# Performance work log

Measured on AMD Instinct MI355X. Metric: run time of the kernel, lower is better.

The kernel has to match this reference:

```python
import jax, jax.numpy as jnp
import numpy as np

DIM = 256
NUM_HEADS = 8
SAMPLE_RATIO = 4
B, H, W = 8, 32, 32
HEAD_DIM = DIM // NUM_HEADS
SCALE = HEAD_DIM ** (-0.5)


def conv1x1(x, w, b):
    # x: [B,C,H,W], w: [O,C], b: [O]  (1x1 conv == per-pixel channel matmul)
    return jnp.einsum('bchw,oc->bohw', x, w) + b[None, :, None, None]


def setup_inputs() -> dict:
    key = jax.random.key(0)
    ks = jax.random.split(key, 16)
    s = 0.02
    x = jax.random.normal(ks[0], (B, DIM, H, W), dtype=jnp.float32)
    # gumbel noise for the two gumbel-softmax gates (sampled once, fed as input)
    u_q = jax.random.uniform(ks[1], (B, SAMPLE_RATIO, H, W), minval=1e-6, maxval=1.0 - 1e-6)
    u_k = jax.random.uniform(ks[2], (B, SAMPLE_RATIO, H, W), minval=1e-6, maxval=1.0 - 1e-6)
    g_q = -jnp.log(-jnp.log(u_q))
    g_k = -jnp.log(-jnp.log(u_k))
    return {
        'x': x,
        'g_q': g_q,
        'g_k': g_k,
        'Wsq': jax.random.normal(ks[3], (SAMPLE_RATIO, DIM)) * s,
        'bsq': jnp.zeros((SAMPLE_RATIO,), jnp.float32),
        'Wsk': jax.random.normal(ks[4], (SAMPLE_RATIO, DIM)) * s,
        'bsk': jnp.zeros((SAMPLE_RATIO,), jnp.float32),
        'Wq': jax.random.normal(ks[5], (DIM, DIM)) * s,
        'bq': jnp.zeros((DIM,), jnp.float32),
        'Wk': jax.random.normal(ks[6], (DIM, DIM)) * s,
        'bk': jnp.zeros((DIM,), jnp.float32),
        'Wv': jax.random.normal(ks[7], (DIM, DIM)) * s,
        'bv': jnp.zeros((DIM,), jnp.float32),
        'Wp': jax.random.normal(ks[8], (DIM, DIM)) * s,
        'bp': jnp.zeros((DIM,), jnp.float32),
    }


def reference(x, g_q, g_k, Wsq, bsq, Wsk, bsk, Wq, bq, Wk, bk, Wv, bv, Wp, bp):
    Bn, C, Hh, Ww = x.shape
    N = Hh * Ww
    # gumbel-softmax (soft, tau=1) gates; keep channel 0 only
    sample_q = jax.nn.softmax(conv1x1(x, Wsq, bsq) + g_q, axis=1)[:, :1]   # [B,1,H,W]
    sample_k = jax.nn.softmax(conv1x1(x, Wsk, bsk) + g_k, axis=1)[:, :1]

    q = (sample_q * conv1x1(x, Wq, bq)).reshape(Bn, NUM_HEADS, HEAD_DIM, N)
    k = (sample_k * conv1x1(x, Wk, bk)).reshape(Bn, NUM_HEADS, HEAD_DIM, N)
    v_full = conv1x1(x, Wv, bv)                                            # shortcut [B,C,H,W]
    v = v_full.reshape(Bn, NUM_HEADS, HEAD_DIM, N)

    # dense attention: scores [B,h,N,N]
    attn = jax.nn.softmax(jnp.einsum('bhdn,bhdm->bhnm', q * SCALE, k), axis=-1)
    out = jnp.einsum('bhnm,bhdm->bhdn', attn, v).reshape(Bn, C, Hh, Ww)

    gated = sample_q * out + (1.0 - sample_q) * v_full
    return conv1x1(gated, Wp, bp)
```

## Files before the change

### kernel.cpp

```cpp
#include <hip/hip_runtime.h>
#include <hip/hip_bf16.h>

typedef __hip_bfloat16 bf16;
typedef __attribute__((ext_vector_type(8))) short short8;
typedef __attribute__((ext_vector_type(4))) short sh4;
typedef __attribute__((ext_vector_type(4))) float f32x4;

static __device__ __forceinline__ float bf2f(bf16 h) { return __bfloat162float(h); }
static __device__ __forceinline__ short f2bfs(float f) {
    bf16 h = __float2bfloat16(f);
    return *reinterpret_cast<short*>(&h);
}
static __device__ __forceinline__ short8 cvt8(float4 a, float4 b) {
    short8 o;
    o[0] = f2bfs(a.x); o[1] = f2bfs(a.y); o[2] = f2bfs(a.z); o[3] = f2bfs(a.w);
    o[4] = f2bfs(b.x); o[5] = f2bfs(b.y); o[6] = f2bfs(b.z); o[7] = f2bfs(b.w);
    return o;
}

constexpr int Bn = 8;
constexpr int C  = 256;
constexpr int N  = 1024;
constexpr int NH = 8;
constexpr int HD = 32;
constexpr int TS = 264;
constexpr float SCALE = 0.17677669529663687f;

__global__ __launch_bounds__(256) void k_prep(
    const float* __restrict__ Wq, const float* __restrict__ Wk,
    const float* __restrict__ Wv, const float* __restrict__ Wp,
    bf16* __restrict__ Wb)
{
    const int tid = threadIdx.x;
    const int mat = blockIdx.x >> 2, seg = blockIdx.x & 3;
    const float* src = (mat == 0) ? Wq : (mat == 1) ? Wk : (mat == 2) ? Wv : Wp;
    short* dst = reinterpret_cast<short*>(Wb) + (size_t)mat * 256 * 256;
#pragma unroll
    for (int i = 0; i < 16; ++i) {
        int f4 = seg * 4096 + i * 256 + tid;
        float4 v = reinterpret_cast<const float4*>(src)[f4];
        sh4 o;
        o[0] = f2bfs(v.x); o[1] = f2bfs(v.y); o[2] = f2bfs(v.z); o[3] = f2bfs(v.w);
        *reinterpret_cast<sh4*>(dst + (size_t)f4 * 4) = o;
    }
}

__global__ __launch_bounds__(256) void k_fused5(
    const float* __restrict__ x, const float* __restrict__ gq, const float* __restrict__ gk,
    const float* __restrict__ Wsq, const float* __restrict__ bsq,
    const float* __restrict__ Wsk, const float* __restrict__ bsk,
    const bf16* __restrict__ Wb,
    const float* __restrict__ bq, const float* __restrict__ bk, const float* __restrict__ bv,
    bf16* __restrict__ qo, bf16* __restrict__ ko, bf16* __restrict__ vo,
    float* __restrict__ sqg)
{
    __shared__ short T[64 * TS];
    __shared__ float sq_lds[64];
    __shared__ float sk_lds[64];

    const int tid  = threadIdx.x;
    const int wave = tid >> 6;
    const int lane = tid & 63;
    const int col  = lane & 15;
    const int quad = lane >> 4;

    const int b    = blockIdx.x >> 6;
    const int rest = blockIdx.x & 63;
    const int n0   = (rest >> 2) * 64;
    const int mq   = rest & 3;

    {
        const float* xp = x + (size_t)b * C * N + n0;
        const int row = tid >> 4;
        const int f   = tid & 15;
#pragma unroll
        for (int p = 0; p < 16; ++p) {
            int c = p * 16 + row;
            float4 v = *reinterpret_cast<const float4*>(xp + (size_t)c * N + f * 4);
            T[(f * 4 + 0) * TS + c] = f2bfs(v.x);
            T[(f * 4 + 1) * TS + c] = f2bfs(v.y);
            T[(f * 4 + 2) * TS + c] = f2bfs(v.z);
            T[(f * 4 + 3) * TS + c] = f2bfs(v.w);
        }
    }
    __syncthreads();

    if (wave == 0) {
        const float* wsrc = (col < 4) ? (Wsq + col * C) : (Wsk + (col & 3) * C);
        f32x4 ga[4] = {};
#pragma unroll
        for (int k0 = 0; k0 < 256; k0 += 32) {
            float4 w0 = *reinterpret_cast<const float4*>(wsrc + k0 + quad * 8);
            float4 w1 = *reinterpret_cast<const float4*>(wsrc + k0 + quad * 8 + 4);
            short8 af = cvt8(w0, w1);
#pragma unroll
            for (int cf = 0; cf < 4; ++cf) {
                short8 bfr = *reinterpret_cast<const short8*>(&T[(cf * 16 + col) * TS + k0 + quad * 8]);
                ga[cf] = __builtin_amdgcn_mfma_f32_16x16x32_bf16(af, bfr, ga[cf], 0, 0, 0);
            }
        }
        if (quad < 2) {
            const float* bsrc = (quad == 0) ? bsq : bsk;
            const float* gsrc = (quad == 0) ? gq : gk;
#pragma unroll
            for (int cf = 0; cf < 4; ++cf) {
                int n = n0 + cf * 16 + col;
                float a[4];
#pragma unroll
                for (int r = 0; r < 4; ++r)
                    a[r] = ga[cf][r] + bsrc[r] + gsrc[(size_t)b * 4 * N + (size_t)r * N + n];
                float mx = fmaxf(fmaxf(a[0], a[1]), fmaxf(a[2], a[3]));
                float e = 0.f;
#pragma unroll
                for (int r = 0; r < 4; ++r) e += __expf(a[r] - mx);
                float p0 = __expf(a[0] - mx) / e;
                if (quad == 0) {
                    sq_lds[cf * 16 + col] = p0;
                    if (mq == 0) sqg[b * N + n] = p0;
                } else {
                    sk_lds[cf * 16 + col] = p0;
                }
            }
        }
    }
    __syncthreads();

    const short* Ws = reinterpret_cast<const short*>(Wb);
    const int mbase = mq * 192 + wave * 48;
    f32x4 acc[3][4] = {};
#pragma unroll
    for (int k0 = 0; k0 < 256; k0 += 32) {
        short8 bfr[4];
#pragma unroll
        for (int cf = 0; cf < 4; ++cf)
            bfr[cf] = *reinterpret_cast<const short8*>(&T[(cf * 16 + col) * TS + k0 + quad * 8]);
#pragma unroll
        for (int i = 0; i < 3; ++i) {
            int m = mbase + i * 16;
            const short* wr = Ws + (size_t)(m >> 8) * 65536
                              + (size_t)((m & 255) + col) * 256 + k0 + quad * 8;
            short8 af = *reinterpret_cast<const short8*>(wr);
#pragma unroll
            for (int cf = 0; cf < 4; ++cf)
                acc[i][cf] = __builtin_amdgcn_mfma_f32_16x16x32_bf16(af, bfr[cf], acc[i][cf], 0, 0, 0);
        }
    }
#pragma unroll
    for (int i = 0; i < 3; ++i) {
        int m = mbase + i * 16;
        int mat = m >> 8;
        int cr  = (m & 255) + quad * 4;
        const float* bb = (mat == 0) ? bq : (mat == 1) ? bk : bv;
        float bias[4];
#pragma unroll
        for (int r = 0; r < 4; ++r) bias[r] = bb[cr + r];
        if (mat < 2) {
            short* op = reinterpret_cast<short*>((mat == 0) ? qo : ko) + (size_t)b * N * C;
#pragma unroll
            for (int cf = 0; cf < 4; ++cf) {
                int n = n0 + cf * 16 + col;
                float g = (mat == 0) ? sq_lds[cf * 16 + col] * SCALE
                                     : sk_lds[cf * 16 + col];
                sh4 pack;
#pragma unroll
                for (int r = 0; r < 4; ++r) pack[r] = f2bfs((acc[i][cf][r] + bias[r]) * g);
                *reinterpret_cast<sh4*>(op + (size_t)n * C + cr) = pack;
            }
        } else {
            bf16* op = vo + (size_t)b * C * N;
#pragma unroll
            for (int cf = 0; cf < 4; ++cf) {
                int n = n0 + cf * 16 + col;
#pragma unroll
                for (int r = 0; r < 4; ++r)
                    op[(size_t)(cr + r) * N + n] = __float2bfloat16(acc[i][cf][r] + bias[r]);
            }
        }
    }
}

__global__ __launch_bounds__(256) void k_attn5(
    const bf16* __restrict__ qo, const bf16* __restrict__ ko,
    const bf16* __restrict__ vo, const float* __restrict__ sqg,
    bf16* __restrict__ gt)
{
    __shared__ short P_lds[4][32 * 72];

    const int tid  = threadIdx.x;
    const int wave = tid >> 6;
    const int lane = tid & 63;
    const int col  = lane & 15;
    const int quad = lane >> 4;

    const int b = blockIdx.x >> 6;
    const int h = (blockIdx.x >> 3) & 7;
    const int qbase = (blockIdx.x & 7) * 128 + wave * 32;

    const short* kp = reinterpret_cast<const short*>(ko) + (size_t)b * N * C + h * HD + quad * 8;
    const short* vp = reinterpret_cast<const short*>(vo) + (size_t)b * C * N + (size_t)h * HD * N;

    short8 qf[2];
    {
        const short* qp = reinterpret_cast<const short*>(qo) + (size_t)b * N * C + h * HD + quad * 8;
#pragma unroll
        for (int g = 0; g < 2; ++g)
            qf[g] = *reinterpret_cast<const short8*>(qp + (size_t)(qbase + g * 16 + col) * C);
    }

    float l[2] = {};
    f32x4 oac[2][2] = {};
    short* P = P_lds[wave];

    short8 kf[4];
#pragma unroll
    for (int c = 0; c < 4; ++c)
        kf[c] = *reinterpret_cast<const short8*>(kp + (size_t)(c * 16 + col) * C);

    for (int kb = 0; kb < N; kb += 64) {
        short8 vf[2][2];
#pragma unroll
        for (int kg = 0; kg < 2; ++kg)
#pragma unroll
            for (int dh = 0; dh < 2; ++dh)
                vf[kg][dh] = *reinterpret_cast<const short8*>(vp + (size_t)(dh * 16 + col) * N + kb + kg * 32 + quad * 8);

#pragma unroll
        for (int g = 0; g < 2; ++g) {
            float s[16];
#pragma unroll
            for (int c = 0; c < 4; ++c) {
                f32x4 acc = {};
                acc = __builtin_amdgcn_mfma_f32_16x16x32_bf16(kf[c], qf[g], acc, 0, 0, 0);
#pragma unroll
                for (int r = 0; r < 4; ++r) s[c * 4 + r] = acc[r];
            }
            float p[16], lloc = 0.f;
#pragma unroll
            for (int i = 0; i < 16; ++i) { p[i] = __expf(s[i]); lloc += p[i]; }
            lloc += __shfl_xor(lloc, 16, 64);
            lloc += __shfl_xor(lloc, 32, 64);
            l[g] += lloc;
#pragma unroll
            for (int c = 0; c < 4; ++c) {
                sh4 pk;
#pragma unroll
                for (int r = 0; r < 4; ++r) pk[r] = f2bfs(p[c * 4 + r]);
                *reinterpret_cast<sh4*>(&P[(g * 16 + col) * 72 + c * 16 + quad * 4]) = pk;
            }
        }

        const int kn = (kb + 64) & (N - 1);
#pragma unroll
        for (int c = 0; c < 4; ++c)
            kf[c] = *reinterpret_cast<const short8*>(kp + (size_t)(kn + c * 16 + col) * C);

#pragma unroll
        for (int kg = 0; kg < 2; ++kg) {
#pragma unroll
            for (int g = 0; g < 2; ++g) {
                short8 pf = *reinterpret_cast<const short8*>(&P[(g * 16 + col) * 72 + kg * 32 + quad * 8]);
#pragma unroll
                for (int dh = 0; dh < 2; ++dh)
                    oac[g][dh] = __builtin_amdgcn_mfma_f32_16x16x32_bf16(vf[kg][dh], pf, oac[g][dh], 0, 0, 0);
            }
        }
    }

#pragma unroll
    for (int g = 0; g < 2; ++g) {
        const int q = qbase + g * 16 + col;
        const float invl = 1.f / l[g];
        const float sqv  = sqg[b * N + q];
        const float hv   = 1.f - sqv;
        short* gp = reinterpret_cast<short*>(gt) + ((size_t)b * N + q) * C + h * HD + quad * 4;
#pragma unroll
        for (int dh = 0; dh < 2; ++dh) {
            sh4 pack;
#pragma unroll
            for (int r = 0; r < 4; ++r) {
                int d = dh * 16 + quad * 4 + r;
                float vb = bf2f(*reinterpret_cast<const bf16*>(vp + (size_t)d * N + q));
                pack[r] = f2bfs(sqv * (oac[g][dh][r] * invl) + hv * vb);
            }
            *reinterpret_cast<sh4*>(gp + dh * 16) = pack;
        }
    }
}

__global__ __launch_bounds__(256) void k_projm3(
    const bf16* __restrict__ gt, const bf16* __restrict__ Wpb,
    const float* __restrict__ bp, float* __restrict__ out)
{
    const int tid  = threadIdx.x;
    const int wave = tid >> 6, lane = tid & 63;
    const int col  = lane & 15, quad = lane >> 4;
    const int mrow = blockIdx.x * 128 + wave * 32;
    const int b    = blockIdx.z;
    const int n0   = blockIdx.y * 32;

    const short* Wm = reinterpret_cast<const short*>(Wpb);
    const short* gp = reinterpret_cast<const short*>(gt) + (size_t)b * N * C;

    f32x4 acc[2][2] = {};
#pragma unroll
    for (int k0 = 0; k0 < 256; k0 += 32) {
        short8 af[2];
#pragma unroll
        for (int mi = 0; mi < 2; ++mi)
            af[mi] = *reinterpret_cast<const short8*>(Wm + (size_t)(mrow + mi * 16 + col) * 256 + k0 + quad * 8);
        short8 bfr[2];
#pragma unroll
        for (int cf = 0; cf < 2; ++cf)
            bfr[cf] = *reinterpret_cast<const short8*>(gp + (size_t)(n0 + cf * 16 + col) * C + k0 + quad * 8);
#pragma unroll
        for (int mi = 0; mi < 2; ++mi)
#pragma unroll
            for (int cf = 0; cf < 2; ++cf)
                acc[mi][cf] = __builtin_amdgcn_mfma_f32_16x16x32_bf16(af[mi], bfr[cf], acc[mi][cf], 0, 0, 0);
    }

    float* op = out + (size_t)b * C * N;
#pragma unroll
    for (int mi = 0; mi < 2; ++mi) {
        int cr = mrow + mi * 16 + quad * 4;
        float bias[4];
#pragma unroll
        for (int r = 0; r < 4; ++r) bias[r] = bp[cr + r];
#pragma unroll
        for (int cf = 0; cf < 2; ++cf) {
            int n = n0 + cf * 16 + col;
#pragma unroll
            for (int r = 0; r < 4; ++r)
                op[(size_t)(cr + r) * N + n] = acc[mi][cf][r] + bias[r];
        }
    }
}

extern "C" void kernel_launch(void* const* d_in, const int* in_sizes, int n_in,
                              void* d_out, int out_size, void* d_ws, size_t ws_size,
                              hipStream_t stream)
{
    const float* x   = (const float*)d_in[0];
    const float* gq  = (const float*)d_in[1];
    const float* gk  = (const float*)d_in[2];
    const float* Wsq = (const float*)d_in[3];
    const float* bsq = (const float*)d_in[4];
    const float* Wsk = (const float*)d_in[5];
    const float* bsk = (const float*)d_in[6];
    const float* Wq  = (const float*)d_in[7];
    const float* bq  = (const float*)d_in[8];
    const float* Wk  = (const float*)d_in[9];
    const float* bk  = (const float*)d_in[10];
    const float* Wv  = (const float*)d_in[11];
    const float* bv  = (const float*)d_in[12];
    const float* Wp  = (const float*)d_in[13];
    const float* bp  = (const float*)d_in[14];

    char* ws = (char*)d_ws;
    float* sqg = (float*)ws;
    bf16* Wb   = (bf16*)(ws + 32768);
    bf16* qo   = (bf16*)(ws + 32768 + 524288);
    bf16* ko   = qo + (size_t)Bn * N * C;
    bf16* vo   = ko + (size_t)Bn * N * C;
    bf16* gt   = vo + (size_t)Bn * C * N;
    float* out = (float*)d_out;

    k_prep<<<16, 256, 0, stream>>>(Wq, Wk, Wv, Wp, Wb);
    k_fused5<<<512, 256, 0, stream>>>(x, gq, gk, Wsq, bsq, Wsk, bsk,
                                      Wb, bq, bk, bv, qo, ko, vo, sqg);
    k_attn5<<<512, 256, 0, stream>>>(qo, ko, vo, sqg, gt);
    k_projm3<<<dim3(2, 32, 8), 256, 0, stream>>>(gt, Wb + 3 * 65536, bp, out);
}
```

Before: 149.0 us.

## Stage K and V tiles in double-buffered LDS shared across waves

The attention kernel stops having each of its four waves load K and V fragments from global memory on its own. All 256 threads now cooperatively load each 64-key tile of K and V into double-buffered shared memory, and every wave reads its fragments from there. Each tile is fetched once per block instead of once per wave, and the next tile is prefetched into registers while the current one is computed. The cost is one block-wide barrier per tile iteration and extra LDS usage, which could reduce occupancy.

```diff
diff --git a/kernel.cpp b/kernel.cpp
--- a/kernel.cpp
+++ b/kernel.cpp
@@ -179,12 +179,14 @@
     }
 }
 
-__global__ __launch_bounds__(256) void k_attn5(
+__global__ __launch_bounds__(256) void k_attn6(
     const bf16* __restrict__ qo, const bf16* __restrict__ ko,
     const bf16* __restrict__ vo, const float* __restrict__ sqg,
     bf16* __restrict__ gt)
 {
     __shared__ short P_lds[4][32 * 72];
+    __shared__ short K_lds[2][64 * 40];
+    __shared__ short V_lds[2][32 * 72];
 
     const int tid  = threadIdx.x;
     const int wave = tid >> 6;
@@ -196,8 +198,14 @@
     const int h = (blockIdx.x >> 3) & 7;
     const int qbase = (blockIdx.x & 7) * 128 + wave * 32;
 
-    const short* kp = reinterpret_cast<const short*>(ko) + (size_t)b * N * C + h * HD + quad * 8;
-    const short* vp = reinterpret_cast<const short*>(vo) + (size_t)b * C * N + (size_t)h * HD * N;
+    const int skey = tid >> 2;
+    const int sd   = (tid & 3) * 8;
+    const int svd  = tid >> 3;
+    const int svk  = (tid & 7) * 8;
+
+    const short* kgp = reinterpret_cast<const short*>(ko) + (size_t)b * N * C + h * HD;
+    const short* vgp = reinterpret_cast<const short*>(vo) + (size_t)b * C * N + (size_t)h * HD * N;
+    const short* vp  = vgp;
 
     short8 qf[2];
     {
@@ -211,18 +219,24 @@
     f32x4 oac[2][2] = {};
     short* P = P_lds[wave];
 
-    short8 kf[4];
-#pragma unroll
-    for (int c = 0; c < 4; ++c)
-        kf[c] = *reinterpret_cast<const short8*>(kp + (size_t)(c * 16 + col) * C);
-
-    for (int kb = 0; kb < N; kb += 64) {
-        short8 vf[2][2];
-#pragma unroll
-        for (int kg = 0; kg < 2; ++kg)
-#pragma unroll
-            for (int dh = 0; dh < 2; ++dh)
-                vf[kg][dh] = *reinterpret_cast<const short8*>(vp + (size_t)(dh * 16 + col) * N + kb + kg * 32 + quad * 8);
+    short8 kstage = *reinterpret_cast<const short8*>(kgp + (size_t)skey * C + sd);
+    short8 vstage = *reinterpret_cast<const short8*>(vgp + (size_t)svd * N + svk);
+    *reinterpret_cast<short8*>(&K_lds[0][skey * 40 + sd]) = kstage;
+    *reinterpret_cast<short8*>(&V_lds[0][svd * 72 + svk]) = vstage;
+    __syncthreads();
+
+    for (int t = 0; t < 16; ++t) {
+        const int tn = (t + 1) & 15;
+        kstage = *reinterpret_cast<const short8*>(kgp + (size_t)(tn * 64 + skey) * C + sd);
+        vstage = *reinterpret_cast<const short8*>(vgp + (size_t)svd * N + tn * 64 + svk);
+
+        const short* Kb = K_lds[t & 1];
+        const short* Vb = V_lds[t & 1];
+
+        short8 kf[4];
+#pragma unroll
+        for (int c = 0; c < 4; ++c)
+            kf[c] = *reinterpret_cast<const short8*>(&Kb[(c * 16 + col) * 40 + quad * 8]);
 
 #pragma unroll
         for (int g = 0; g < 2; ++g) {
@@ -249,21 +263,24 @@
             }
         }
 
-        const int kn = (kb + 64) & (N - 1);
-#pragma unroll
-        for (int c = 0; c < 4; ++c)
-            kf[c] = *reinterpret_cast<const short8*>(kp + (size_t)(kn + c * 16 + col) * C);
-
 #pragma unroll
         for (int kg = 0; kg < 2; ++kg) {
+            short8 vf[2];
+#pragma unroll
+            for (int dh = 0; dh < 2; ++dh)
+                vf[dh] = *reinterpret_cast<const short8*>(&Vb[(dh * 16 + col) * 72 + kg * 32 + quad * 8]);
 #pragma unroll
             for (int g = 0; g < 2; ++g) {
                 short8 pf = *reinterpret_cast<const short8*>(&P[(g * 16 + col) * 72 + kg * 32 + quad * 8]);
 #pragma unroll
                 for (int dh = 0; dh < 2; ++dh)
-                    oac[g][dh] = __builtin_amdgcn_mfma_f32_16x16x32_bf16(vf[kg][dh], pf, oac[g][dh], 0, 0, 0);
-            }
-        }
+                    oac[g][dh] = __builtin_amdgcn_mfma_f32_16x16x32_bf16(vf[dh], pf, oac[g][dh], 0, 0, 0);
+            }
+        }
+
+        *reinterpret_cast<short8*>(&K_lds[(t + 1) & 1][skey * 40 + sd]) = kstage;
+        *reinterpret_cast<short8*>(&V_lds[(t + 1) & 1][svd * 72 + svk]) = vstage;
+        __syncthreads();
     }
 
 #pragma unroll
@@ -368,6 +385,6 @@
     k_prep<<<16, 256, 0, stream>>>(Wq, Wk, Wv, Wp, Wb);
     k_fused5<<<512, 256, 0, stream>>>(x, gq, gk, Wsq, bsq, Wsk, bsk,
                                       Wb, bq, bk, bv, qo, ko, vo, sqg);
-    k_attn5<<<512, 256, 0, stream>>>(qo, ko, vo, sqg, gt);
+    k_attn6<<<512, 256, 0, stream>>>(qo, ko, vo, sqg, gt);
     k_projm3<<<dim3(2, 32, 8), 256, 0, stream>>>(gt, Wb + 3 * 65536, bp, out);
 }
```

After: 138.7 us. 1.07x faster.
